# Performance work log

Hardware: AMD Instinct MI355X
Metric: run time of the kernel (lower is better)

The kernel has to match this reference:

```python
import jax, jax.numpy as jnp
import numpy as np

B, C, H, W = 2048, 256, 7, 7
EPS = 1e-6  # torch.nn.CosineSimilarity eps


def _masked_cos_loss(f1, f2, A):
    """Fused all-pairs masked cosine similarity.
    f1, f2: [B, C, H, W]; A: [H, W, H, W] binary mask.
    Replaces the original 7x7x7x7 Python loop of per-pixel CosineSimilarity calls.
    Returns per-batch loss [B]: sum_{ijkl: A==1} cos(f1[:,:,i,j], f2[:,:,k,l]) / (H*W*H*W).
    """
    n1 = jnp.linalg.norm(f1, axis=1)  # [B, H, W]
    n2 = jnp.linalg.norm(f2, axis=1)  # [B, H, W]
    dot = jnp.einsum('bcij,bckl->bijkl', f1, f2)  # [B, H, W, H, W]
    denom = jnp.maximum(n1[:, :, :, None, None] * n2[:, None, None, :, :], EPS)
    cos = dot / denom
    mask = (A == 1).astype(f1.dtype)
    return jnp.einsum('bijkl,ijkl->b', cos, mask) / (H * W * H * W)


def setup_inputs() -> dict:
    key = jax.random.key(0)
    k1, k2, k3, k4 = jax.random.split(key, 4)
    base_feature = jax.random.normal(k1, (B, C, H, W), dtype=jnp.float32)
    moment_feature = jax.random.normal(k2, (B, C, H, W), dtype=jnp.float32)
    base_A = jax.random.randint(k3, (H, W, H, W), 0, 2, dtype=jnp.int32)
    moment_A = jax.random.randint(k4, (H, W, H, W), 0, 2, dtype=jnp.int32)
    return {"base_feature": base_feature, "moment_feature": moment_feature,
            "base_A": base_A, "moment_A": moment_A}


def reference(base_feature, moment_feature, base_A, moment_A):
    # base_loss  = masked cos(base[i,j],   moment[k,l]) under base_A
    # moment_loss = masked cos(moment[i,j], base[k,l])  under moment_A
    base_loss = _masked_cos_loss(base_feature, moment_feature, base_A)
    moment_loss = _masked_cos_loss(moment_feature, base_feature, moment_A)
    return -base_loss - moment_loss  # [B]
```

## Files before the change

### kernel.cpp

```cpp
#include <hip/hip_runtime.h>
#include <math.h>


constexpr int NB     = 2048;
constexpr int NC     = 256;
constexpr int NP     = 49;
constexpr int SLAB_C = 4;
constexpr int FW     = NP * SLAB_C;
constexpr int BUFW   = 2 * FW;
constexpr int REGION = 1280;
constexpr int NSLABW = (NC / 2) / SLAB_C;
constexpr float EPS  = 1e-6f;

__global__ __launch_bounds__(256, 2)
void pixpro_kernel(const float* __restrict__ gbase,
                   const float* __restrict__ gmom,
                   const int*   __restrict__ A1,
                   const int*   __restrict__ A2,
                   float*       __restrict__ out)
{
    __shared__ unsigned char wtb[NP * NP];
    __shared__ __align__(16) float slab[4][REGION];

    const int tid  = threadIdx.x;
    const int wave = tid >> 6;
    const int lane = tid & 63;
    const int b    = blockIdx.x * 2 + (wave >> 1);
    const int half = wave & 1;

    for (int t = tid; t < NP * NP; t += 256) {
        int p = t / NP, q = t - p * NP;
        wtb[t] = (unsigned char)((A1[t] == 1 ? 1 : 0) + (A2[q * NP + p] == 1 ? 1 : 0));
    }
    __syncthreads();

    float* const sl = slab[wave];

    const int lp = lane & 7, lq = lane >> 3;
    const int p0 = (lp < 7 ? lp : 6) * 7;
    const int q0 = (lq < 7 ? lq : 6) * 7;

    const float* gb = gbase + (size_t)b * (NC * NP) + (size_t)half * (128 * NP);
    const float* gm = gmom  + (size_t)b * (NC * NP) + (size_t)half * (128 * NP);
    const float* gbl = gb + lane;
    const float* gml = gm + lane;

    const bool ld = (lane < NP);

    const int vAw = (lane < NP) ? (4 * lane) : (FW + 4 * (lane - NP));
    const int vBw = FW + 4 * ((lane < 34) ? (15 + lane) : 48);

    float acc[7][7];
    #pragma unroll
    for (int j = 0; j < 7; ++j)
        #pragma unroll
        for (int i = 0; i < 7; ++i) acc[j][i] = 0.0f;
    float nrm0 = 0.0f, nrm1 = 0.0f;

    float4 pbA = {}, pmA = {}, pbB = {}, pmB = {};
    if (ld) {
        pbA.x = gbl[0];      pbA.y = gbl[NP];      pbA.z = gbl[2 * NP];      pbA.w = gbl[3 * NP];
        pmA.x = gml[0];      pmA.y = gml[NP];      pmA.z = gml[2 * NP];      pmA.w = gml[3 * NP];
        pbB.x = gbl[FW];     pbB.y = gbl[FW + NP]; pbB.z = gbl[FW + 2 * NP]; pbB.w = gbl[FW + 3 * NP];
        pmB.x = gml[FW];     pmB.y = gml[FW + NP]; pmB.z = gml[FW + 2 * NP]; pmB.w = gml[FW + 3 * NP];
    }

    auto compute = [&](int Boff) {
        const float* base_ = sl + Boff;
        float4 a4 = *(const float4*)(base_ + vAw);
        float4 b4 = *(const float4*)(base_ + vBw);
        nrm0 = fmaf(a4.x, a4.x, fmaf(a4.y, a4.y, fmaf(a4.z, a4.z, fmaf(a4.w, a4.w, nrm0))));
        nrm1 = fmaf(b4.x, b4.x, fmaf(b4.y, b4.y, fmaf(b4.z, b4.z, fmaf(b4.w, b4.w, nrm1))));
        float4 mv[7];
        #pragma unroll
        for (int j = 0; j < 7; ++j)
            mv[j] = *(const float4*)(base_ + FW + q0 * 4 + 4 * j);
        #pragma unroll
        for (int i = 0; i < 7; ++i) {
            float4 bv = *(const float4*)(base_ + p0 * 4 + 4 * i);
            #pragma unroll
            for (int j = 0; j < 7; ++j) {
                float t0 = fmaf(bv.x, mv[j].x, acc[j][i]);
                t0       = fmaf(bv.y, mv[j].y, t0);
                t0       = fmaf(bv.z, mv[j].z, t0);
                acc[j][i] = fmaf(bv.w, mv[j].w, t0);
            }
        }
    };

    for (int s = 0; s < NSLABW; s += 2) {
        if (ld) {
            *(float4*)(sl + 4 * lane)      = pbA;
            *(float4*)(sl + FW + 4 * lane) = pmA;
            if (s + 2 < NSLABW) {
                const float* pb_ = gbl + (s + 2) * FW;
                const float* pm_ = gml + (s + 2) * FW;
                pbA.x = pb_[0]; pbA.y = pb_[NP]; pbA.z = pb_[2 * NP]; pbA.w = pb_[3 * NP];
                pmA.x = pm_[0]; pmA.y = pm_[NP]; pmA.z = pm_[2 * NP]; pmA.w = pm_[3 * NP];
            }
        }
        asm volatile("s_waitcnt lgkmcnt(0)" ::: "memory");
        compute(0);

        if (ld) {
            *(float4*)(sl + BUFW + 4 * lane)      = pbB;
            *(float4*)(sl + BUFW + FW + 4 * lane) = pmB;
            if (s + 3 < NSLABW) {
                const float* pb_ = gbl + (s + 3) * FW;
                const float* pm_ = gml + (s + 3) * FW;
                pbB.x = pb_[0]; pbB.y = pb_[NP]; pbB.z = pb_[2 * NP]; pbB.w = pb_[3 * NP];
                pmB.x = pm_[0]; pmB.y = pm_[NP]; pmB.z = pm_[2 * NP]; pmB.w = pm_[3 * NP];
            }
        }
        asm volatile("s_waitcnt lgkmcnt(0)" ::: "memory");
        compute(BUFW);
    }

    __syncthreads();

    float* const ex   = slab[wave & ~1];
    const bool active = (lp < 7) && (lq < 7);
    const int  tix    = lq * 7 + lp;

    if (half) {
        ex[lane]      = nrm0;
        ex[64 + lane] = nrm1;
        if (active) {
            #pragma unroll
            for (int j = 0; j < 7; ++j)
                #pragma unroll
                for (int i = 0; i < 7; ++i)
                    ex[128 + tix * 49 + j * 7 + i] = acc[j][i];
        }
    }
    __syncthreads();

    if (!half) {
        nrm0 += ex[lane];
        nrm1 += ex[64 + lane];
        if (active) {
            #pragma unroll
            for (int j = 0; j < 7; ++j)
                #pragma unroll
                for (int i = 0; i < 7; ++i)
                    acc[j][i] += ex[128 + tix * 49 + j * 7 + i];
        }
        asm volatile("s_waitcnt lgkmcnt(0)" ::: "memory");

        ex[lane] = nrm0;
        if (lane < 34) ex[64 + lane] = nrm1;
        asm volatile("s_waitcnt lgkmcnt(0)" ::: "memory");

        float nbv[7], nmv[7];
        #pragma unroll
        for (int i = 0; i < 7; ++i) nbv[i] = sqrtf(ex[p0 + i]);
        #pragma unroll
        for (int j = 0; j < 7; ++j) nmv[j] = sqrtf(ex[NP + q0 + j]);

        float sum = 0.0f;
        if (active) {
            #pragma unroll
            for (int j = 0; j < 7; ++j)
                #pragma unroll
                for (int i = 0; i < 7; ++i) {
                    float w     = (float)wtb[(p0 + i) * NP + (q0 + j)];
                    float denom = fmaxf(nbv[i] * nmv[j], EPS);
                    sum += w * acc[j][i] / denom;
                }
        }
        #pragma unroll
        for (int m = 32; m; m >>= 1) sum += __shfl_xor(sum, m, 64);
        if (lane == 0) out[b] = sum * (-1.0f / 2401.0f);
    }
}

extern "C" void kernel_launch(void* const* d_in, const int* in_sizes, int n_in,
                              void* d_out, int out_size, void* d_ws, size_t ws_size,
                              hipStream_t stream)
{
    (void)in_sizes; (void)n_in; (void)d_ws; (void)ws_size; (void)out_size;
    const float* base = (const float*)d_in[0];
    const float* mom  = (const float*)d_in[1];
    const int*   A1   = (const int*)d_in[2];
    const int*   A2   = (const int*)d_in[3];
    float*       out  = (float*)d_out;

    pixpro_kernel<<<NB / 2, 256, 0, stream>>>(base, mom, A1, A2, out);
}
```

Baseline: 248.4 us.

## Use one batch per 128-thread block with deeper register prefetch pipeline

Each block now handles one batch element with two waves, one per channel half, instead of two batches with four waves. Global loads are spread across all 64 lanes and prefetched four slabs ahead in registers, which is meant to hide more memory latency. The cross-wave reduction of the 7x7x49 accumulators is split into two passes so it fits in the smaller shared memory region. The cost is an extra pair of barriers in the epilogue and more live registers for the prefetch buffers.

New measurement: 534.0 us. +115.0%, slower.

```diff
diff --git a/kernel.cpp b/kernel.cpp
--- a/kernel.cpp
+++ b/kernel.cpp
@@ -8,11 +8,11 @@
 constexpr int SLAB_C = 4;
 constexpr int FW     = NP * SLAB_C;
 constexpr int BUFW   = 2 * FW;
-constexpr int REGION = 1280;
+constexpr int WREG   = 2 * BUFW;
 constexpr int NSLABW = (NC / 2) / SLAB_C;
 constexpr float EPS  = 1e-6f;
 
-__global__ __launch_bounds__(256, 2)
+__global__ __launch_bounds__(128, 2)
 void pixpro_kernel(const float* __restrict__ gbase,
                    const float* __restrict__ gmom,
                    const int*   __restrict__ A1,
@@ -20,15 +20,15 @@
                    float*       __restrict__ out)
 {
     __shared__ unsigned char wtb[NP * NP];
-    __shared__ __align__(16) float slab[4][REGION];
+    __shared__ __align__(16) float slab[2][WREG];
 
     const int tid  = threadIdx.x;
     const int wave = tid >> 6;
     const int lane = tid & 63;
-    const int b    = blockIdx.x * 2 + (wave >> 1);
-    const int half = wave & 1;
-
-    for (int t = tid; t < NP * NP; t += 256) {
+    const int b    = blockIdx.x;
+    const int half = wave;
+
+    for (int t = tid; t < NP * NP; t += 128) {
         int p = t / NP, q = t - p * NP;
         wtb[t] = (unsigned char)((A1[t] == 1 ? 1 : 0) + (A2[q * NP + p] == 1 ? 1 : 0));
     }
@@ -42,13 +42,28 @@
 
     const float* gb = gbase + (size_t)b * (NC * NP) + (size_t)half * (128 * NP);
     const float* gm = gmom  + (size_t)b * (NC * NP) + (size_t)half * (128 * NP);
-    const float* gbl = gb + lane;
-    const float* gml = gm + lane;
-
-    const bool ld = (lane < NP);
-
-    const int vAw = (lane < NP) ? (4 * lane) : (FW + 4 * (lane - NP));
-    const int vBw = FW + 4 * ((lane < 34) ? (15 + lane) : 48);
+
+    const bool  is_b = (lane < NP);
+    const bool  has1 = (lane < 34);
+    const float* gi0 = is_b ? (gb + lane) : (gm + (lane - NP));
+    const float* gi1 = gm + 15 + (has1 ? lane : 0);
+
+    const int w0 = is_b ? (4 * lane) : (FW + 4 * (lane - NP));
+    const int w1 = FW + 4 * (has1 ? (15 + lane) : 48);
+
+#define LOADSET(R0, R1, s) do {                                            \
+        const float* _p0 = gi0 + (s) * (SLAB_C * NP);                      \
+        R0.x = _p0[0]; R0.y = _p0[NP]; R0.z = _p0[2*NP]; R0.w = _p0[3*NP]; \
+        if (has1) {                                                        \
+            const float* _p1 = gi1 + (s) * (SLAB_C * NP);                  \
+            R1.x = _p1[0]; R1.y = _p1[NP]; R1.z = _p1[2*NP]; R1.w = _p1[3*NP]; \
+        }                                                                  \
+    } while (0)
+
+#define WRITESET(R0, R1, boff) do {                                        \
+        *(float4*)(sl + (boff) + w0) = R0;                                 \
+        if (has1) *(float4*)(sl + (boff) + w1) = R1;                       \
+    } while (0)
 
     float acc[7][7];
     #pragma unroll
@@ -57,27 +72,19 @@
         for (int i = 0; i < 7; ++i) acc[j][i] = 0.0f;
     float nrm0 = 0.0f, nrm1 = 0.0f;
 
-    float4 pbA = {}, pmA = {}, pbB = {}, pmB = {};
-    if (ld) {
-        pbA.x = gbl[0];      pbA.y = gbl[NP];      pbA.z = gbl[2 * NP];      pbA.w = gbl[3 * NP];
-        pmA.x = gml[0];      pmA.y = gml[NP];      pmA.z = gml[2 * NP];      pmA.w = gml[3 * NP];
-        pbB.x = gbl[FW];     pbB.y = gbl[FW + NP]; pbB.z = gbl[FW + 2 * NP]; pbB.w = gbl[FW + 3 * NP];
-        pmB.x = gml[FW];     pmB.y = gml[FW + NP]; pmB.z = gml[FW + 2 * NP]; pmB.w = gml[FW + 3 * NP];
-    }
-
-    auto compute = [&](int Boff) {
+    auto compute = [&](const int Boff) {
         const float* base_ = sl + Boff;
-        float4 a4 = *(const float4*)(base_ + vAw);
-        float4 b4 = *(const float4*)(base_ + vBw);
+        float4 a4 = *(const float4*)(base_ + w0);
+        float4 b4 = *(const float4*)(base_ + w1);
         nrm0 = fmaf(a4.x, a4.x, fmaf(a4.y, a4.y, fmaf(a4.z, a4.z, fmaf(a4.w, a4.w, nrm0))));
         nrm1 = fmaf(b4.x, b4.x, fmaf(b4.y, b4.y, fmaf(b4.z, b4.z, fmaf(b4.w, b4.w, nrm1))));
         float4 mv[7];
         #pragma unroll
         for (int j = 0; j < 7; ++j)
-            mv[j] = *(const float4*)(base_ + FW + q0 * 4 + 4 * j);
+            mv[j] = *(const float4*)(base_ + FW + 4 * (q0 + j));
         #pragma unroll
         for (int i = 0; i < 7; ++i) {
-            float4 bv = *(const float4*)(base_ + p0 * 4 + 4 * i);
+            float4 bv = *(const float4*)(base_ + 4 * (p0 + i));
             #pragma unroll
             for (int j = 0; j < 7; ++j) {
                 float t0 = fmaf(bv.x, mv[j].x, acc[j][i]);
@@ -88,37 +95,35 @@
         }
     };
 
-    for (int s = 0; s < NSLABW; s += 2) {
-        if (ld) {
-            *(float4*)(sl + 4 * lane)      = pbA;
-            *(float4*)(sl + FW + 4 * lane) = pmA;
-            if (s + 2 < NSLABW) {
-                const float* pb_ = gbl + (s + 2) * FW;
-                const float* pm_ = gml + (s + 2) * FW;
-                pbA.x = pb_[0]; pbA.y = pb_[NP]; pbA.z = pb_[2 * NP]; pbA.w = pb_[3 * NP];
-                pmA.x = pm_[0]; pmA.y = pm_[NP]; pmA.z = pm_[2 * NP]; pmA.w = pm_[3 * NP];
-            }
-        }
-        asm volatile("s_waitcnt lgkmcnt(0)" ::: "memory");
+    float4 a0f = {}, a1f = {}, b0f = {}, b1f = {};
+    float4 c0f = {}, c1f = {}, d0f = {}, d1f = {};
+    LOADSET(a0f, a1f, 0);
+    LOADSET(b0f, b1f, 1);
+    LOADSET(c0f, c1f, 2);
+    LOADSET(d0f, d1f, 3);
+    WRITESET(a0f, a1f, 0);
+    LOADSET(a0f, a1f, 4);
+
+    for (int s4 = 0; s4 < NSLABW; s4 += 4) {
+        if (s4 + 1 < NSLABW) WRITESET(b0f, b1f, BUFW);
+        if (s4 + 5 < NSLABW) LOADSET(b0f, b1f, s4 + 5);
         compute(0);
-
-        if (ld) {
-            *(float4*)(sl + BUFW + 4 * lane)      = pbB;
-            *(float4*)(sl + BUFW + FW + 4 * lane) = pmB;
-            if (s + 3 < NSLABW) {
-                const float* pb_ = gbl + (s + 3) * FW;
-                const float* pm_ = gml + (s + 3) * FW;
-                pbB.x = pb_[0]; pbB.y = pb_[NP]; pbB.z = pb_[2 * NP]; pbB.w = pb_[3 * NP];
-                pmB.x = pm_[0]; pmB.y = pm_[NP]; pmB.z = pm_[2 * NP]; pmB.w = pm_[3 * NP];
-            }
-        }
-        asm volatile("s_waitcnt lgkmcnt(0)" ::: "memory");
+        if (s4 + 2 < NSLABW) WRITESET(c0f, c1f, 0);
+        if (s4 + 6 < NSLABW) LOADSET(c0f, c1f, s4 + 6);
         compute(BUFW);
-    }
-
-    __syncthreads();
-
-    float* const ex   = slab[wave & ~1];
+        if (s4 + 3 < NSLABW) WRITESET(d0f, d1f, BUFW);
+        if (s4 + 7 < NSLABW) LOADSET(d0f, d1f, s4 + 7);
+        compute(0);
+        if (s4 + 4 < NSLABW) WRITESET(a0f, a1f, 0);
+        if (s4 + 8 < NSLABW) LOADSET(a0f, a1f, s4 + 8);
+        compute(BUFW);
+    }
+
+#undef LOADSET
+#undef WRITESET
+
+    __syncthreads();
+    float* const ex   = &slab[0][0];
     const bool active = (lp < 7) && (lq < 7);
     const int  tix    = lq * 7 + lp;
 
@@ -127,26 +132,42 @@
         ex[64 + lane] = nrm1;
         if (active) {
             #pragma unroll
-            for (int j = 0; j < 7; ++j)
+            for (int j = 0; j < 4; ++j)
                 #pragma unroll
                 for (int i = 0; i < 7; ++i)
-                    ex[128 + tix * 49 + j * 7 + i] = acc[j][i];
-        }
-    }
-    __syncthreads();
-
+                    ex[128 + tix * 28 + j * 7 + i] = acc[j][i];
+        }
+    }
+    __syncthreads();
     if (!half) {
         nrm0 += ex[lane];
         nrm1 += ex[64 + lane];
         if (active) {
             #pragma unroll
-            for (int j = 0; j < 7; ++j)
+            for (int j = 0; j < 4; ++j)
                 #pragma unroll
                 for (int i = 0; i < 7; ++i)
-                    acc[j][i] += ex[128 + tix * 49 + j * 7 + i];
-        }
-        asm volatile("s_waitcnt lgkmcnt(0)" ::: "memory");
-
+                    acc[j][i] += ex[128 + tix * 28 + j * 7 + i];
+        }
+    }
+    __syncthreads();
+    if (half && active) {
+        #pragma unroll
+        for (int j = 4; j < 7; ++j)
+            #pragma unroll
+            for (int i = 0; i < 7; ++i)
+                ex[tix * 21 + (j - 4) * 7 + i] = acc[j][i];
+    }
+    __syncthreads();
+
+    if (!half) {
+        if (active) {
+            #pragma unroll
+            for (int j = 4; j < 7; ++j)
+                #pragma unroll
+                for (int i = 0; i < 7; ++i)
+                    acc[j][i] += ex[tix * 21 + (j - 4) * 7 + i];
+        }
         ex[lane] = nrm0;
         if (lane < 34) ex[64 + lane] = nrm1;
         asm volatile("s_waitcnt lgkmcnt(0)" ::: "memory");
@@ -185,5 +206,5 @@
     const int*   A2   = (const int*)d_in[3];
     float*       out  = (float*)d_out;
 
-    pixpro_kernel<<<NB / 2, 256, 0, stream>>>(base, mom, A1, A2, out);
+    pixpro_kernel<<<NB, 128, 0, stream>>>(base, mom, A1, A2, out);
 }
```
